# Performance work log

Measured on AMD Instinct MI355X. Metric: run time of the kernel, lower is better.

## Reference

```python
import jax, jax.numpy as jnp
import numpy as np

N_EMBD = 1024
N_EXPERTS = 8
TOP_K = 2
D_FF = 4 * N_EMBD


def setup_inputs() -> dict:
    key = jax.random.key(0)
    ks = jax.random.split(key, 6)
    B, S = 4, 2048
    s = 1.0 / np.sqrt(N_EMBD)
    sf = 1.0 / np.sqrt(D_FF)
    x = jax.random.normal(ks[0], (B, S, N_EMBD), dtype=jnp.float32)
    router_w = jax.random.uniform(ks[1], (N_EMBD, N_EXPERTS), minval=-s, maxval=s, dtype=jnp.float32)
    wfc = jax.random.uniform(ks[2], (N_EXPERTS, N_EMBD, D_FF), minval=-s, maxval=s, dtype=jnp.float32)
    bfc = jax.random.uniform(ks[3], (N_EXPERTS, D_FF), minval=-s, maxval=s, dtype=jnp.float32)
    wproj = jax.random.uniform(ks[4], (N_EXPERTS, D_FF, N_EMBD), minval=-sf, maxval=sf, dtype=jnp.float32)
    bproj = jax.random.uniform(ks[5], (N_EXPERTS, N_EMBD), minval=-sf, maxval=sf, dtype=jnp.float32)
    return {"x": x, "router_w": router_w, "wfc": wfc, "bfc": bfc, "wproj": wproj, "bproj": bproj}


def reference(x, router_w, wfc, bfc, wproj, bproj):
    B, S, D = x.shape
    E = wfc.shape[0]
    xf = x.reshape(-1, D)  # [N, D] tokens
    logits = xf @ router_w  # [N, E]
    probs = jax.nn.softmax(logits.astype(jnp.float32), axis=-1)
    w, sel = jax.lax.top_k(probs, TOP_K)  # [N, K]
    w = w / jnp.sum(w, axis=-1, keepdims=True)  # norm_topk_prob
    w = w.astype(x.dtype)
    out = jnp.zeros_like(xf)
    for e in range(E):
        # per-token gate for expert e (0 if not routed here) -- same math as
        # gather -> MLP -> weighted scatter-add in the original
        gate = jnp.sum(jnp.where(sel == e, w, jnp.zeros_like(w)), axis=-1)  # [N]
        h = jax.nn.gelu(xf @ wfc[e] + bfc[e], approximate=False)  # [N, 4D]
        y = h @ wproj[e] + bproj[e]  # [N, D]
        out = out + gate[:, None] * y
    return out.reshape(B, S, D)
```

## Files before the change

kernel.cpp:

```cpp
#include <hip/hip_runtime.h>
#include <hip/hip_bf16.h>


#define N_TOK 8192
#define DMODEL 1024
#define NEXP 8
#define DFF 4096
#define CAP 8192

typedef __attribute__((ext_vector_type(8))) short short8;
typedef __attribute__((ext_vector_type(4))) float f32x4;

#define GLOAD_LDS16(g, l)                                              \
  __builtin_amdgcn_global_load_lds(                                    \
      (const __attribute__((address_space(1))) unsigned int*)(g),      \
      (__attribute__((address_space(3))) unsigned int*)(l), 16, 0, 0)

__device__ __forceinline__ unsigned short f2bf(float f) {
  unsigned u = __float_as_uint(f);
  return (unsigned short)((u + 0x7FFFu + ((u >> 16) & 1u)) >> 16);
}

__device__ __forceinline__ float gelu_f(float v) {
  return 0.5f * v * (1.0f + erff(v * 0.70710678118654752f));
}

__device__ __forceinline__ short8 pack8(float f0, float f1, float f2, float f3,
                                        float f4, float f5, float f6, float f7) {
  short8 r;
  r[0] = (short)f2bf(f0); r[1] = (short)f2bf(f1);
  r[2] = (short)f2bf(f2); r[3] = (short)f2bf(f3);
  r[4] = (short)f2bf(f4); r[5] = (short)f2bf(f5);
  r[6] = (short)f2bf(f6); r[7] = (short)f2bf(f7);
  return r;
}

__global__ void router_k(const float* __restrict__ x, const float* __restrict__ rw,
                         int* __restrict__ cnt, int* __restrict__ tok,
                         float* __restrict__ gate) {
  int lane = threadIdx.x & 63;
  int t = blockIdx.x * 4 + (threadIdx.x >> 6);
  const float* xr = x + (size_t)t * DMODEL;
  float p[8];
#pragma unroll
  for (int e = 0; e < 8; ++e) p[e] = 0.0f;
#pragma unroll
  for (int j = 0; j < DMODEL / 64; ++j) {
    int i = lane + j * 64;
    float xv = xr[i];
    const float4* r = (const float4*)(rw + (size_t)i * 8);
    float4 a = r[0], b = r[1];
    p[0] += xv * a.x; p[1] += xv * a.y; p[2] += xv * a.z; p[3] += xv * a.w;
    p[4] += xv * b.x; p[5] += xv * b.y; p[6] += xv * b.z; p[7] += xv * b.w;
  }
#pragma unroll
  for (int e = 0; e < 8; ++e) {
#pragma unroll
    for (int off = 32; off; off >>= 1) p[e] += __shfl_xor(p[e], off, 64);
  }
  if (lane == 0) {
    int e1 = 0;
#pragma unroll
    for (int e = 1; e < 8; ++e) if (p[e] > p[e1]) e1 = e;
    int e2 = (e1 == 0) ? 1 : 0;
#pragma unroll
    for (int e = 0; e < 8; ++e) if (e != e1 && p[e] > p[e2]) e2 = e;
    float w1 = 1.0f / (1.0f + expf(p[e2] - p[e1]));
    float w2 = 1.0f - w1;
    int s1 = atomicAdd(&cnt[e1], 1);
    tok[e1 * CAP + s1] = t; gate[e1 * CAP + s1] = w1;
    int s2 = atomicAdd(&cnt[e2], 1);
    tok[e2 * CAP + s2] = t; gate[e2 * CAP + s2] = w2;
  }
}

__global__ void prefix_k(const int* __restrict__ cnt, int* __restrict__ off) {
  if (threadIdx.x == 0 && blockIdx.x == 0) {
    int s = 0;
    for (int e = 0; e < NEXP; ++e) { off[e] = s; s += cnt[e]; }
  }
}

__global__ void cvt_x_k(const float* __restrict__ x, unsigned short* __restrict__ xb) {
  int i = (blockIdx.x * 256 + threadIdx.x) * 8;
  const float4* p = (const float4*)(x + i);
  float4 a = p[0], b = p[1];
  *(short8*)(xb + i) = pack8(a.x, a.y, a.z, a.w, b.x, b.y, b.z, b.w);
}

__global__ __launch_bounds__(256) void cvt_wt_k(const float* __restrict__ W,
                                                unsigned short* __restrict__ WT,
                                                int K, int N) {
  __shared__ float ls[64][68];
  int b = blockIdx.x;
  int nkt = K >> 6, nnt = N >> 6;
  int kt = b % nkt;
  int nt = (b / nkt) % nnt;
  int e = b / (nkt * nnt);
  const float* Wb = W + (size_t)e * K * N + (size_t)(kt * 64) * N + nt * 64;
  int t = threadIdx.x;
  int nn = (t & 15) * 4, kr = t >> 4;
#pragma unroll
  for (int i = 0; i < 4; ++i) {
    float4 v = *(const float4*)(Wb + (size_t)(kr + 16 * i) * N + nn);
    *(float4*)&ls[kr + 16 * i][nn] = v;
  }
  __syncthreads();
  int on = t >> 2, kc = (t & 3) * 16;
  unsigned short* dst = WT + (size_t)e * N * K + (size_t)(nt * 64 + on) * K + kt * 64 + kc;
  short8 r0, r1;
#pragma unroll
  for (int j = 0; j < 8; ++j) r0[j] = (short)f2bf(ls[kc + j][on]);
#pragma unroll
  for (int j = 0; j < 8; ++j) r1[j] = (short)f2bf(ls[kc + 8 + j][on]);
  *(short8*)dst = r0;
  *(short8*)(dst + 8) = r1;
}

__global__ __launch_bounds__(256, 4) void gemm1a_k(
    const unsigned short* __restrict__ xb, const unsigned short* __restrict__ wT,
    const float* __restrict__ bfc, const int* __restrict__ cnt,
    const int* __restrict__ off, const int* __restrict__ tok,
    unsigned short* __restrict__ h) {
  int bid = (int)(blockIdx.x & 7) * ((int)gridDim.x >> 3) + (int)(blockIdx.x >> 3);
  int mt = bid & 63;
  int nt = (bid >> 6) & 31;
  int e = bid >> 11;
  int Me = cnt[e];
  if (mt * 128 >= Me) return;
  int base = off[e];
  int n0 = nt * 128;

  __shared__ __align__(16) unsigned short As[128 * 32];
  __shared__ __align__(16) unsigned short Bs[128 * 32];

  int tid = threadIdx.x;
  int lane = tid & 63, w = tid >> 6;
  int lr = lane >> 2;
  int lc = (lane & 3) * 8;

  int ar0i = mt * 128 + w * 32 + lr;
  int ar1i = ar0i + 16;
  int t0 = tok[e * CAP + ((ar0i < Me) ? ar0i : (Me - 1))];
  int t1 = tok[e * CAP + ((ar1i < Me) ? ar1i : (Me - 1))];
  const unsigned short* gA0 = xb + (size_t)t0 * DMODEL + lc;
  const unsigned short* gA1 = xb + (size_t)t1 * DMODEL + lc;
  const unsigned short* gB0 = wT + ((size_t)e * DFF + n0 + w * 32 + lr) * DMODEL + lc;
  const unsigned short* gB1 = gB0 + (size_t)16 * DMODEL;
  unsigned short* lA0 = &As[(w * 32) * 32];
  unsigned short* lA1 = &As[(w * 32 + 16) * 32];
  unsigned short* lB0 = &Bs[(w * 32) * 32];
  unsigned short* lB1 = &Bs[(w * 32 + 16) * 32];

  int wr = w >> 1, wc = w & 1;
  int g = lane >> 4, fr = lane & 15;

  f32x4 acc[4][4];
#pragma unroll
  for (int i = 0; i < 4; ++i)
#pragma unroll
    for (int j = 0; j < 4; ++j) acc[i][j] = (f32x4)0.0f;

#pragma unroll 1
  for (int k0 = 0; k0 < DMODEL; k0 += 32) {
    GLOAD_LDS16(gA0 + k0, lA0);
    GLOAD_LDS16(gA1 + k0, lA1);
    GLOAD_LDS16(gB0 + k0, lB0);
    GLOAD_LDS16(gB1 + k0, lB1);
    __syncthreads();
    short8 af[4], bfv[4];
#pragma unroll
    for (int i = 0; i < 4; ++i) af[i] = *(const short8*)&As[(wr * 64 + i * 16 + fr) * 32 + g * 8];
#pragma unroll
    for (int i = 0; i < 4; ++i) bfv[i] = *(const short8*)&Bs[(wc * 64 + i * 16 + fr) * 32 + g * 8];
#pragma unroll
    for (int mi = 0; mi < 4; ++mi)
#pragma unroll
      for (int ni = 0; ni < 4; ++ni)
        acc[mi][ni] = __builtin_amdgcn_mfma_f32_16x16x32_bf16(af[mi], bfv[ni], acc[mi][ni], 0, 0, 0);
    __syncthreads();
  }

#pragma unroll
  for (int mi = 0; mi < 4; ++mi) {
    int rl = wr * 64 + mi * 16 + g * 4;
#pragma unroll
    for (int i = 0; i < 4; ++i) {
      int r = mt * 128 + rl + i;
      if (r < Me) {
        unsigned short* hrow = h + (size_t)(base + r) * DFF;
#pragma unroll
        for (int ni = 0; ni < 4; ++ni) {
          int col = n0 + wc * 64 + ni * 16 + fr;
          float v = acc[mi][ni][i] + bfc[e * DFF + col];
          hrow[col] = f2bf(gelu_f(v));
        }
      }
    }
  }
}

__global__ __launch_bounds__(256, 4) void gemm2a_k(
    const unsigned short* __restrict__ h, const unsigned short* __restrict__ wT,
    const float* __restrict__ bproj, const int* __restrict__ cnt,
    const int* __restrict__ off, const int* __restrict__ tok,
    const float* __restrict__ gate, float* __restrict__ out) {
  int bid = (int)(blockIdx.x & 7) * ((int)gridDim.x >> 3) + (int)(blockIdx.x >> 3);
  int mt = bid & 63;
  int nt = (bid >> 6) & 7;
  int e = bid >> 9;
  int Me = cnt[e];
  if (mt * 128 >= Me) return;
  int base = off[e];
  int n0 = nt * 128;

  __shared__ __align__(16) unsigned short As[128 * 32];
  __shared__ __align__(16) unsigned short Bs[128 * 32];

  int tid = threadIdx.x;
  int lane = tid & 63, w = tid >> 6;
  int lr = lane >> 2;
  int lc = (lane & 3) * 8;

  const unsigned short* gA0 = h + (size_t)(base + mt * 128 + w * 32 + lr) * DFF + lc;
  const unsigned short* gA1 = gA0 + (size_t)16 * DFF;
  const unsigned short* gB0 = wT + ((size_t)e * DMODEL + n0 + w * 32 + lr) * DFF + lc;
  const unsigned short* gB1 = gB0 + (size_t)16 * DFF;
  unsigned short* lA0 = &As[(w * 32) * 32];
  unsigned short* lA1 = &As[(w * 32 + 16) * 32];
  unsigned short* lB0 = &Bs[(w * 32) * 32];
  unsigned short* lB1 = &Bs[(w * 32 + 16) * 32];

  int wr = w >> 1, wc = w & 1;
  int g = lane >> 4, fr = lane & 15;

  f32x4 acc[4][4];
#pragma unroll
  for (int i = 0; i < 4; ++i)
#pragma unroll
    for (int j = 0; j < 4; ++j) acc[i][j] = (f32x4)0.0f;

#pragma unroll 1
  for (int k0 = 0; k0 < DFF; k0 += 32) {
    GLOAD_LDS16(gA0 + k0, lA0);
    GLOAD_LDS16(gA1 + k0, lA1);
    GLOAD_LDS16(gB0 + k0, lB0);
    GLOAD_LDS16(gB1 + k0, lB1);
    __syncthreads();
    short8 af[4], bfv[4];
#pragma unroll
    for (int i = 0; i < 4; ++i) af[i] = *(const short8*)&As[(wr * 64 + i * 16 + fr) * 32 + g * 8];
#pragma unroll
    for (int i = 0; i < 4; ++i) bfv[i] = *(const short8*)&Bs[(wc * 64 + i * 16 + fr) * 32 + g * 8];
#pragma unroll
    for (int mi = 0; mi < 4; ++mi)
#pragma unroll
      for (int ni = 0; ni < 4; ++ni)
        acc[mi][ni] = __builtin_amdgcn_mfma_f32_16x16x32_bf16(af[mi], bfv[ni], acc[mi][ni], 0, 0, 0);
    __syncthreads();
  }

#pragma unroll
  for (int mi = 0; mi < 4; ++mi) {
    int rl = wr * 64 + mi * 16 + g * 4;
#pragma unroll
    for (int i = 0; i < 4; ++i) {
      int r = mt * 128 + rl + i;
      if (r < Me) {
        int tkn = tok[e * CAP + r];
        float gv = gate[e * CAP + r];
        float* orow = out + (size_t)tkn * DMODEL;
#pragma unroll
        for (int ni = 0; ni < 4; ++ni) {
          int col = n0 + wc * 64 + ni * 16 + fr;
          float v = acc[mi][ni][i] + bproj[e * DMODEL + col];
          atomicAdd(orow + col, gv * v);
        }
      }
    }
  }
}

extern "C" void kernel_launch(void* const* d_in, const int* in_sizes, int n_in,
                              void* d_out, int out_size, void* d_ws, size_t ws_size,
                              hipStream_t stream) {
  const float* x = (const float*)d_in[0];
  const float* rw = (const float*)d_in[1];
  const float* wfc = (const float*)d_in[2];
  const float* bfc = (const float*)d_in[3];
  const float* wproj = (const float*)d_in[4];
  const float* bproj = (const float*)d_in[5];
  float* out = (float*)d_out;

  char* ws = (char*)d_ws;
  int* cnt = (int*)ws;
  int* off_ = (int*)(ws + 64);
  int* tok = (int*)(ws + 4096);
  float* gate = (float*)(ws + 4096 + (size_t)NEXP * CAP * 4);
  size_t HOFF = 4096 + 2 * (size_t)NEXP * CAP * 4;
  unsigned short* h = (unsigned short*)(ws + HOFF);
  size_t HSZ = (size_t)(16384 + 128) * DFF * 2;
  size_t XOFF = HOFF + HSZ;
  size_t WOFF = XOFF + (size_t)N_TOK * DMODEL * 2;
  unsigned short* xb = (unsigned short*)(ws + XOFF);
  unsigned short* wT = (unsigned short*)(ws + WOFF);

  hipMemsetAsync(cnt, 0, 128, stream);
  hipMemsetAsync(out, 0, (size_t)out_size * 4, stream);
  router_k<<<N_TOK / 4, 256, 0, stream>>>(x, rw, cnt, tok, gate);
  prefix_k<<<1, 64, 0, stream>>>(cnt, off_);
  cvt_x_k<<<(N_TOK * DMODEL) / (8 * 256), 256, 0, stream>>>(x, xb);
  cvt_wt_k<<<NEXP * (DMODEL / 64) * (DFF / 64), 256, 0, stream>>>(wfc, wT, DMODEL, DFF);
  gemm1a_k<<<NEXP * 32 * 64, 256, 0, stream>>>(xb, wT, bfc, cnt, off_, tok, h);
  cvt_wt_k<<<NEXP * (DFF / 64) * (DMODEL / 64), 256, 0, stream>>>(wproj, wT, DFF, DMODEL);
  gemm2a_k<<<NEXP * 8 * 64, 256, 0, stream>>>(h, wT, bproj, cnt, off_, tok, gate, out);
}
```

Measured before the change: 820.3 us.

## Double-buffer LDS tiles in expert GEMMs and fuse x bf16 conversion into router

Both expert GEMM kernels now use two LDS buffers, so the global-to-LDS load of the next K slice is issued before the MFMA work on the current slice, overlapping memory latency with compute. This also removes one of the two barriers per K step. Separately, the standalone x-to-bf16 conversion kernel is removed and the router writes the bf16 copy of x while it reads x, saving a launch and a second pass over x. The price is doubled LDS per block (32KB), which may reduce occupancy at the requested 4 blocks per CU, and the router now does scalar 2-byte stores.

```diff
diff --git a/kernel.cpp b/kernel.cpp
--- a/kernel.cpp
+++ b/kernel.cpp
@@ -37,10 +37,11 @@
 
 __global__ void router_k(const float* __restrict__ x, const float* __restrict__ rw,
                          int* __restrict__ cnt, int* __restrict__ tok,
-                         float* __restrict__ gate) {
+                         float* __restrict__ gate, unsigned short* __restrict__ xb) {
   int lane = threadIdx.x & 63;
   int t = blockIdx.x * 4 + (threadIdx.x >> 6);
   const float* xr = x + (size_t)t * DMODEL;
+  unsigned short* xbr = xb + (size_t)t * DMODEL;
   float p[8];
 #pragma unroll
   for (int e = 0; e < 8; ++e) p[e] = 0.0f;
@@ -48,6 +49,7 @@
   for (int j = 0; j < DMODEL / 64; ++j) {
     int i = lane + j * 64;
     float xv = xr[i];
+    xbr[i] = f2bf(xv);
     const float4* r = (const float4*)(rw + (size_t)i * 8);
     float4 a = r[0], b = r[1];
     p[0] += xv * a.x; p[1] += xv * a.y; p[2] += xv * a.z; p[3] += xv * a.w;
@@ -79,13 +81,6 @@
     int s = 0;
     for (int e = 0; e < NEXP; ++e) { off[e] = s; s += cnt[e]; }
   }
-}
-
-__global__ void cvt_x_k(const float* __restrict__ x, unsigned short* __restrict__ xb) {
-  int i = (blockIdx.x * 256 + threadIdx.x) * 8;
-  const float4* p = (const float4*)(x + i);
-  float4 a = p[0], b = p[1];
-  *(short8*)(xb + i) = pack8(a.x, a.y, a.z, a.w, b.x, b.y, b.z, b.w);
 }
 
 __global__ __launch_bounds__(256) void cvt_wt_k(const float* __restrict__ W,
@@ -116,6 +111,33 @@
   *(short8*)dst = r0;
   *(short8*)(dst + 8) = r1;
 }
+
+#define STAGE(buf, kk)                                              \
+  do {                                                              \
+    GLOAD_LDS16(gA0 + (kk), &As[buf][(w * 32 + lr) * 32 + lc]);     \
+    GLOAD_LDS16(gA1 + (kk), &As[buf][(w * 32 + 16 + lr) * 32 + lc]);\
+    GLOAD_LDS16(gB0 + (kk), &Bs[buf][(w * 32 + lr) * 32 + lc]);     \
+    GLOAD_LDS16(gB1 + (kk), &Bs[buf][(w * 32 + 16 + lr) * 32 + lc]);\
+  } while (0)
+
+#define COMPUTE(buf)                                                            \
+  do {                                                                          \
+    short8 af[4], bfv[4];                                                       \
+    _Pragma("unroll") for (int i = 0; i < 4; ++i)                               \
+        af[i] = *(const short8*)&As[buf][(wr * 64 + i * 16 + fr) * 32 + g * 8]; \
+    _Pragma("unroll") for (int i = 0; i < 4; ++i)                               \
+        bfv[i] = *(const short8*)&Bs[buf][(wc * 64 + i * 16 + fr) * 32 + g * 8];\
+    _Pragma("unroll") for (int mi = 0; mi < 4; ++mi)                            \
+        _Pragma("unroll") for (int ni = 0; ni < 4; ++ni)                        \
+            acc[mi][ni] = __builtin_amdgcn_mfma_f32_16x16x32_bf16(              \
+                af[mi], bfv[ni], acc[mi][ni], 0, 0, 0);                         \
+  } while (0)
+
+#define SYNC()                                          \
+  do {                                                  \
+    asm volatile("s_waitcnt vmcnt(0)" ::: "memory");    \
+    __syncthreads();                                    \
+  } while (0)
 
 __global__ __launch_bounds__(256, 4) void gemm1a_k(
     const unsigned short* __restrict__ xb, const unsigned short* __restrict__ wT,
@@ -131,8 +153,8 @@
   int base = off[e];
   int n0 = nt * 128;
 
-  __shared__ __align__(16) unsigned short As[128 * 32];
-  __shared__ __align__(16) unsigned short Bs[128 * 32];
+  __shared__ __align__(16) unsigned short As[2][128 * 32];
+  __shared__ __align__(16) unsigned short Bs[2][128 * 32];
 
   int tid = threadIdx.x;
   int lane = tid & 63, w = tid >> 6;
@@ -147,10 +169,6 @@
   const unsigned short* gA1 = xb + (size_t)t1 * DMODEL + lc;
   const unsigned short* gB0 = wT + ((size_t)e * DFF + n0 + w * 32 + lr) * DMODEL + lc;
   const unsigned short* gB1 = gB0 + (size_t)16 * DMODEL;
-  unsigned short* lA0 = &As[(w * 32) * 32];
-  unsigned short* lA1 = &As[(w * 32 + 16) * 32];
-  unsigned short* lB0 = &Bs[(w * 32) * 32];
-  unsigned short* lB1 = &Bs[(w * 32 + 16) * 32];
 
   int wr = w >> 1, wc = w & 1;
   int g = lane >> 4, fr = lane & 15;
@@ -161,24 +179,16 @@
 #pragma unroll
     for (int j = 0; j < 4; ++j) acc[i][j] = (f32x4)0.0f;
 
+  STAGE(0, 0);
+  SYNC();
 #pragma unroll 1
-  for (int k0 = 0; k0 < DMODEL; k0 += 32) {
-    GLOAD_LDS16(gA0 + k0, lA0);
-    GLOAD_LDS16(gA1 + k0, lA1);
-    GLOAD_LDS16(gB0 + k0, lB0);
-    GLOAD_LDS16(gB1 + k0, lB1);
-    __syncthreads();
-    short8 af[4], bfv[4];
-#pragma unroll
-    for (int i = 0; i < 4; ++i) af[i] = *(const short8*)&As[(wr * 64 + i * 16 + fr) * 32 + g * 8];
-#pragma unroll
-    for (int i = 0; i < 4; ++i) bfv[i] = *(const short8*)&Bs[(wc * 64 + i * 16 + fr) * 32 + g * 8];
-#pragma unroll
-    for (int mi = 0; mi < 4; ++mi)
-#pragma unroll
-      for (int ni = 0; ni < 4; ++ni)
-        acc[mi][ni] = __builtin_amdgcn_mfma_f32_16x16x32_bf16(af[mi], bfv[ni], acc[mi][ni], 0, 0, 0);
-    __syncthreads();
+  for (int k0 = 0; k0 < DMODEL; k0 += 64) {
+    STAGE(1, k0 + 32);
+    COMPUTE(0);
+    SYNC();
+    if (k0 + 64 < DMODEL) STAGE(0, k0 + 64);
+    COMPUTE(1);
+    SYNC();
   }
 
 #pragma unroll
@@ -214,8 +224,8 @@
   int base = off[e];
   int n0 = nt * 128;
 
-  __shared__ __align__(16) unsigned short As[128 * 32];
-  __shared__ __align__(16) unsigned short Bs[128 * 32];
+  __shared__ __align__(16) unsigned short As[2][128 * 32];
+  __shared__ __align__(16) unsigned short Bs[2][128 * 32];
 
   int tid = threadIdx.x;
   int lane = tid & 63, w = tid >> 6;
@@ -226,10 +236,6 @@
   const unsigned short* gA1 = gA0 + (size_t)16 * DFF;
   const unsigned short* gB0 = wT + ((size_t)e * DMODEL + n0 + w * 32 + lr) * DFF + lc;
   const unsigned short* gB1 = gB0 + (size_t)16 * DFF;
-  unsigned short* lA0 = &As[(w * 32) * 32];
-  unsigned short* lA1 = &As[(w * 32 + 16) * 32];
-  unsigned short* lB0 = &Bs[(w * 32) * 32];
-  unsigned short* lB1 = &Bs[(w * 32 + 16) * 32];
 
   int wr = w >> 1, wc = w & 1;
   int g = lane >> 4, fr = lane & 15;
@@ -240,24 +246,16 @@
 #pragma unroll
     for (int j = 0; j < 4; ++j) acc[i][j] = (f32x4)0.0f;
 
+  STAGE(0, 0);
+  SYNC();
 #pragma unroll 1
-  for (int k0 = 0; k0 < DFF; k0 += 32) {
-    GLOAD_LDS16(gA0 + k0, lA0);
-    GLOAD_LDS16(gA1 + k0, lA1);
-    GLOAD_LDS16(gB0 + k0, lB0);
-    GLOAD_LDS16(gB1 + k0, lB1);
-    __syncthreads();
-    short8 af[4], bfv[4];
-#pragma unroll
-    for (int i = 0; i < 4; ++i) af[i] = *(const short8*)&As[(wr * 64 + i * 16 + fr) * 32 + g * 8];
-#pragma unroll
-    for (int i = 0; i < 4; ++i) bfv[i] = *(const short8*)&Bs[(wc * 64 + i * 16 + fr) * 32 + g * 8];
-#pragma unroll
-    for (int mi = 0; mi < 4; ++mi)
-#pragma unroll
-      for (int ni = 0; ni < 4; ++ni)
-        acc[mi][ni] = __builtin_amdgcn_mfma_f32_16x16x32_bf16(af[mi], bfv[ni], acc[mi][ni], 0, 0, 0);
-    __syncthreads();
+  for (int k0 = 0; k0 < DFF; k0 += 64) {
+    STAGE(1, k0 + 32);
+    COMPUTE(0);
+    SYNC();
+    if (k0 + 64 < DFF) STAGE(0, k0 + 64);
+    COMPUTE(1);
+    SYNC();
   }
 
 #pragma unroll
@@ -307,9 +305,8 @@
 
   hipMemsetAsync(cnt, 0, 128, stream);
   hipMemsetAsync(out, 0, (size_t)out_size * 4, stream);
-  router_k<<<N_TOK / 4, 256, 0, stream>>>(x, rw, cnt, tok, gate);
+  router_k<<<N_TOK / 4, 256, 0, stream>>>(x, rw, cnt, tok, gate, xb);
   prefix_k<<<1, 64, 0, stream>>>(cnt, off_);
-  cvt_x_k<<<(N_TOK * DMODEL) / (8 * 256), 256, 0, stream>>>(x, xb);
   cvt_wt_k<<<NEXP * (DMODEL / 64) * (DFF / 64), 256, 0, stream>>>(wfc, wT, DMODEL, DFF);
   gemm1a_k<<<NEXP * 32 * 64, 256, 0, stream>>>(xb, wT, bfc, cnt, off_, tok, h);
   cvt_wt_k<<<NEXP * (DFF / 64) * (DMODEL / 64), 256, 0, stream>>>(wproj, wT, DFF, DMODEL);
```

After: 834.3 us. Within noise of the previous version (+1.7%).
